# Kernel optimization log

Measured on AMD Instinct MI355X. Metric: run time of the kernel, lower is better.

The kernel has to match this reference:

```python
import jax, jax.numpy as jnp
import numpy as np

EMBED_DIM = 64
N_POINTS = 1_000_000


def sinusoidal_embedding(vals, embed_dim):
    # vals: [B] float -> [B, embed_dim]
    half = embed_dim // 2
    log_scale = np.log(10000.0) / (half - 1)
    freqs = jnp.exp(jnp.arange(half, dtype=jnp.float32) * (-log_scale))
    ang = vals[:, None] * freqs[None, :]
    return jnp.concatenate([jnp.sin(ang), jnp.cos(ang)], axis=1)


def embed_mlp(x, w1, b1, w2, b2):
    # Linear -> LeakyReLU(0.1) -> Linear  (embedf / embedm)
    h = jax.nn.leaky_relu(x @ w1.T + b1, negative_slope=0.1)
    return h @ w2.T + b2


def setup_inputs() -> dict:
    key = jax.random.key(0)
    ks = jax.random.split(key, 12)
    d, dh = EMBED_DIM, EMBED_DIM // 2
    s = lambda fan_in: 1.0 / np.sqrt(fan_in)
    return {
        "inputs": jax.random.normal(ks[0], (1, 6, N_POINTS), dtype=jnp.float32),
        "t": jax.random.uniform(ks[1], (1,), dtype=jnp.float32) * 1000.0,
        "mask": jax.random.randint(ks[2], (N_POINTS,), 0, 2, dtype=jnp.int32),
        "pdf": jax.random.normal(ks[3], (N_POINTS, d), dtype=jnp.float32),
        # embedf params: Linear(d,d), Linear(d,d//2)
        "ef_w1": jax.random.uniform(ks[4], (d, d), minval=-s(d), maxval=s(d)),
        "ef_b1": jnp.zeros((d,), jnp.float32),
        "ef_w2": jax.random.uniform(ks[5], (dh, d), minval=-s(d), maxval=s(d)),
        "ef_b2": jnp.zeros((dh,), jnp.float32),
        # embedm params
        "em_w1": jax.random.uniform(ks[6], (d, d), minval=-s(d), maxval=s(d)),
        "em_b1": jnp.zeros((d,), jnp.float32),
        "em_w2": jax.random.uniform(ks[7], (dh, d), minval=-s(d), maxval=s(d)),
        "em_b2": jnp.zeros((dh,), jnp.float32),
    }


def reference(inputs, t, mask, pdf, ef_w1, ef_b1, ef_w2, ef_b2, em_w1, em_b1, em_w2, em_b2):
    n = inputs.shape[-1]
    # pdf branch: [N, 64] -> [1, 64, N]
    pdf_cnl = pdf.T[None]  # [1, 64, N]
    # timestep embedding -> embedf -> broadcast over points
    te = embed_mlp(sinusoidal_embedding(t, EMBED_DIM), ef_w1, ef_b1, ef_w2, ef_b2)  # [1, 32]
    temb = jnp.broadcast_to(te[:, :, None], (te.shape[0], te.shape[1], n))  # [1, 32, N]
    # per-point mask embedding -> embedm
    me = embed_mlp(sinusoidal_embedding(mask.astype(jnp.float32), EMBED_DIM), em_w1, em_b1, em_w2, em_b2)  # [N, 32]
    memb = me.T[None]  # [1, 32, N]
    temb = jnp.concatenate([temb, memb], axis=1)  # [1, 64, N]
    # return conditioning tensors produced by the (truncated) forward prefix
    return jnp.concatenate([pdf_cnl, temb], axis=1)  # [1, 128, N]
```

## Files before the change

kernel.cpp:

```cpp
#include <hip/hip_runtime.h>
#include <math.h>


#define HALF 32

__global__ void embed_small_kernel(const float* __restrict__ t,
                                   const float* __restrict__ ef_w1, const float* __restrict__ ef_b1,
                                   const float* __restrict__ ef_w2, const float* __restrict__ ef_b2,
                                   const float* __restrict__ em_w1, const float* __restrict__ em_b1,
                                   const float* __restrict__ em_w2, const float* __restrict__ em_b2,
                                   float* __restrict__ ws) {
    __shared__ float h[3][64];
    const int tid = threadIdx.x;
    const float log_scale = 0.2970934777f;

    if (tid < 192) {
        const int v = tid / 64;
        const int j = tid % 64;
        const float val = (v == 0) ? t[0] : (float)(v - 1);
        const float* w1 = (v == 0) ? ef_w1 : em_w1;
        const float* b1 = (v == 0) ? ef_b1 : em_b1;
        float acc = b1[j];
        for (int k = 0; k < HALF; ++k) {
            float f = expf(-(float)k * log_scale);
            float ang = val * f;
            float s, c;
            sincosf(ang, &s, &c);
            acc += s * w1[j * 64 + k] + c * w1[j * 64 + HALF + k];
        }
        h[v][j] = (acc > 0.0f) ? acc : 0.1f * acc;
    }
    __syncthreads();
    if (tid < 96) {
        const int v = tid / 32;
        const int c = tid % 32;
        const float* w2 = (v == 0) ? ef_w2 : em_w2;
        const float* b2 = (v == 0) ? ef_b2 : em_b2;
        float acc = b2[c];
        const float* hh = h[v];
        for (int j = 0; j < 64; ++j) acc += hh[j] * w2[c * 64 + j];
        ws[v * 32 + c] = acc;
    }
}

__global__ __launch_bounds__(256) void pvcnn_cond_kernel(
        const float* __restrict__ pdf,
        const int* __restrict__ mask,
        const float* __restrict__ ws,
        float* __restrict__ out,
        int N) {
    __shared__ float tile[64][65];
    __shared__ float emb[96];

    const int tid = threadIdx.x;
    const long long p0 = (long long)blockIdx.x * 64;
    const bool full = (p0 + 64 <= (long long)N);

    if (tid < 96) emb[tid] = ws[tid];

    if (full) {
        const float4* pdf4 = (const float4*)(pdf + p0 * 64);
        #pragma unroll
        for (int it = 0; it < 4; ++it) {
            int f = tid + it * 256;
            int p = f >> 4;
            int q = f & 15;
            float4 v = pdf4[p * 16 + q];
            tile[p][4 * q + 0] = v.x;
            tile[p][4 * q + 1] = v.y;
            tile[p][4 * q + 2] = v.z;
            tile[p][4 * q + 3] = v.w;
        }
    } else {
        #pragma unroll
        for (int it = 0; it < 4; ++it) {
            int f = tid + it * 256;
            int p = f >> 4;
            int q = f & 15;
            float4 v = make_float4(0.f, 0.f, 0.f, 0.f);
            if (p0 + p < (long long)N) {
                const float4* pdf4 = (const float4*)(pdf + (p0 + p) * 64);
                v = pdf4[q];
            }
            tile[p][4 * q + 0] = v.x;
            tile[p][4 * q + 1] = v.y;
            tile[p][4 * q + 2] = v.z;
            tile[p][4 * q + 3] = v.w;
        }
    }

    const int p = tid & 63;
    const int wv = tid >> 6;
    const bool pok = (p0 + p < (long long)N);
    int mval = 0;
    if (pok) mval = mask[p0 + p];

    __syncthreads();

    if (pok) {
        const long long col = p0 + p;
        #pragma unroll
        for (int cb = 0; cb < 64; cb += 4) {
            int c = cb + wv;
            out[(long long)c * N + col] = tile[p][c];
        }
        #pragma unroll
        for (int cb = 0; cb < 32; cb += 4) {
            int c = cb + wv;
            out[(long long)(64 + c) * N + col] = emb[c];
        }
        #pragma unroll
        for (int cb = 0; cb < 32; cb += 4) {
            int c = cb + wv;
            out[(long long)(96 + c) * N + col] = mval ? emb[64 + c] : emb[32 + c];
        }
    }
}

extern "C" void kernel_launch(void* const* d_in, const int* in_sizes, int n_in,
                              void* d_out, int out_size, void* d_ws, size_t ws_size,
                              hipStream_t stream) {
    const float* t     = (const float*)d_in[1];
    const int*   mask  = (const int*)d_in[2];
    const float* pdf   = (const float*)d_in[3];
    const float* ef_w1 = (const float*)d_in[4];
    const float* ef_b1 = (const float*)d_in[5];
    const float* ef_w2 = (const float*)d_in[6];
    const float* ef_b2 = (const float*)d_in[7];
    const float* em_w1 = (const float*)d_in[8];
    const float* em_b1 = (const float*)d_in[9];
    const float* em_w2 = (const float*)d_in[10];
    const float* em_b2 = (const float*)d_in[11];

    float* out = (float*)d_out;
    float* ws  = (float*)d_ws;
    const int N = in_sizes[2];

    embed_small_kernel<<<1, 192, 0, stream>>>(t, ef_w1, ef_b1, ef_w2, ef_b2,
                                              em_w1, em_b1, em_w2, em_b2, ws);

    const int nblocks = (N + 63) / 64;
    pvcnn_cond_kernel<<<nblocks, 256, 0, stream>>>(pdf, mask, ws, out, N);
}
```

Measured before the change: 163.2 us.

## Widen transpose tile to 256 points and emit float4 stores per row

Each block now handles 256 points instead of 64. The pdf tile uses a padded column-major LDS layout so that each thread can read 4 consecutive points of a channel as a float4. Output writes, and the mask reads on the fast path, become 128-bit vector accesses, so the store-bound transpose issues fewer, wider memory transactions. LDS use per block grows to about 64KB, which lowers occupancy, and a scalar fallback path is kept for tails and for N not divisible by 4.

```diff
diff --git a/kernel.cpp b/kernel.cpp
--- a/kernel.cpp
+++ b/kernel.cpp
@@ -3,6 +3,12 @@
 
 
 #define HALF 32
+#define TS 256
+
+__device__ __forceinline__ int ldsIdx(int c, int p) {
+    return c * 256 + ((c >> 3) << 2) + p;
+}
+#define TILE_FLOATS 16412
 
 __global__ void embed_small_kernel(const float* __restrict__ t,
                                    const float* __restrict__ ef_w1, const float* __restrict__ ef_b1,
@@ -15,8 +21,8 @@
     const float log_scale = 0.2970934777f;
 
     if (tid < 192) {
-        const int v = tid / 64;
-        const int j = tid % 64;
+        const int v = tid >> 6;
+        const int j = tid & 63;
         const float val = (v == 0) ? t[0] : (float)(v - 1);
         const float* w1 = (v == 0) ? ef_w1 : em_w1;
         const float* b1 = (v == 0) ? ef_b1 : em_b1;
@@ -32,13 +38,12 @@
     }
     __syncthreads();
     if (tid < 96) {
-        const int v = tid / 32;
-        const int c = tid % 32;
+        const int v = tid >> 5;
+        const int c = tid & 31;
         const float* w2 = (v == 0) ? ef_w2 : em_w2;
         const float* b2 = (v == 0) ? ef_b2 : em_b2;
         float acc = b2[c];
-        const float* hh = h[v];
-        for (int j = 0; j < 64; ++j) acc += hh[j] * w2[c * 64 + j];
+        for (int j = 0; j < 64; ++j) acc += h[v][j] * w2[c * 64 + j];
         ws[v * 32 + c] = acc;
     }
 }
@@ -49,70 +54,106 @@
         const float* __restrict__ ws,
         float* __restrict__ out,
         int N) {
-    __shared__ float tile[64][65];
+    __shared__ float tile[TILE_FLOATS];
     __shared__ float emb[96];
 
     const int tid = threadIdx.x;
-    const long long p0 = (long long)blockIdx.x * 64;
-    const bool full = (p0 + 64 <= (long long)N);
+    const long long p0 = (long long)blockIdx.x * TS;
+    const bool fast = (p0 + TS <= (long long)N) && ((N & 3) == 0);
 
     if (tid < 96) emb[tid] = ws[tid];
 
-    if (full) {
-        const float4* pdf4 = (const float4*)(pdf + p0 * 64);
+    if (fast) {
+        const float4* src = (const float4*)(pdf + p0 * 64);
         #pragma unroll
-        for (int it = 0; it < 4; ++it) {
-            int f = tid + it * 256;
-            int p = f >> 4;
-            int q = f & 15;
-            float4 v = pdf4[p * 16 + q];
-            tile[p][4 * q + 0] = v.x;
-            tile[p][4 * q + 1] = v.y;
-            tile[p][4 * q + 2] = v.z;
-            tile[p][4 * q + 3] = v.w;
+        for (int it = 0; it < 16; ++it) {
+            const int f = tid + it * 256;
+            const int p = f >> 4;
+            const int c0 = (f & 15) * 4;
+            const float4 v = src[f];
+            const int b = ldsIdx(c0, p);
+            tile[b + 0 * 256] = v.x;
+            tile[b + 1 * 256] = v.y;
+            tile[b + 2 * 256] = v.z;
+            tile[b + 3 * 256] = v.w;
         }
     } else {
         #pragma unroll
-        for (int it = 0; it < 4; ++it) {
-            int f = tid + it * 256;
-            int p = f >> 4;
-            int q = f & 15;
+        for (int it = 0; it < 16; ++it) {
+            const int f = tid + it * 256;
+            const int p = f >> 4;
+            const int c0 = (f & 15) * 4;
             float4 v = make_float4(0.f, 0.f, 0.f, 0.f);
-            if (p0 + p < (long long)N) {
-                const float4* pdf4 = (const float4*)(pdf + (p0 + p) * 64);
-                v = pdf4[q];
-            }
-            tile[p][4 * q + 0] = v.x;
-            tile[p][4 * q + 1] = v.y;
-            tile[p][4 * q + 2] = v.z;
-            tile[p][4 * q + 3] = v.w;
+            if (p0 + p < (long long)N)
+                v = ((const float4*)(pdf + (p0 + p) * 64))[f & 15];
+            const int b = ldsIdx(c0, p);
+            tile[b + 0 * 256] = v.x;
+            tile[b + 1 * 256] = v.y;
+            tile[b + 2 * 256] = v.z;
+            tile[b + 3 * 256] = v.w;
         }
     }
 
-    const int p = tid & 63;
-    const int wv = tid >> 6;
-    const bool pok = (p0 + p < (long long)N);
-    int mval = 0;
-    if (pok) mval = mask[p0 + p];
+    const int l = tid & 63;
+    const int w = tid >> 6;
+    const long long col = p0 + 4 * l;
+
+    int4 m4 = make_int4(0, 0, 0, 0);
+    if (fast) {
+        m4 = ((const int4*)mask)[(p0 >> 2) + l];
+    } else {
+        if (col + 0 < N) m4.x = mask[col + 0];
+        if (col + 1 < N) m4.y = mask[col + 1];
+        if (col + 2 < N) m4.z = mask[col + 2];
+        if (col + 3 < N) m4.w = mask[col + 3];
+    }
 
     __syncthreads();
 
-    if (pok) {
-        const long long col = p0 + p;
+    if (fast) {
+        float* op = out + (long long)w * N + col;
+        const long long stride = 4LL * N;
         #pragma unroll
-        for (int cb = 0; cb < 64; cb += 4) {
-            int c = cb + wv;
-            out[(long long)c * N + col] = tile[p][c];
+        for (int s = 0; s < 32; ++s) {
+            const int r = 4 * s + w;
+            float4 v;
+            if (s < 16) {
+                v = *(const float4*)&tile[ldsIdx(r, 4 * l)];
+            } else if (s < 24) {
+                const float e = emb[r - 64];
+                v = make_float4(e, e, e, e);
+            } else {
+                const int c = r - 96;
+                const float e0 = emb[32 + c];
+                const float e1 = emb[64 + c];
+                v = make_float4(m4.x ? e1 : e0, m4.y ? e1 : e0,
+                                m4.z ? e1 : e0, m4.w ? e1 : e0);
+            }
+            *(float4*)(op + (long long)s * stride) = v;
         }
-        #pragma unroll
-        for (int cb = 0; cb < 32; cb += 4) {
-            int c = cb + wv;
-            out[(long long)(64 + c) * N + col] = emb[c];
-        }
-        #pragma unroll
-        for (int cb = 0; cb < 32; cb += 4) {
-            int c = cb + wv;
-            out[(long long)(96 + c) * N + col] = mval ? emb[64 + c] : emb[32 + c];
+    } else {
+        for (int s = 0; s < 32; ++s) {
+            const int r = 4 * s + w;
+            float vals[4];
+            if (s < 16) {
+                #pragma unroll
+                for (int j = 0; j < 4; ++j) vals[j] = tile[ldsIdx(r, 4 * l + j)];
+            } else if (s < 24) {
+                const float e = emb[r - 64];
+                vals[0] = vals[1] = vals[2] = vals[3] = e;
+            } else {
+                const int c = r - 96;
+                const float e0 = emb[32 + c];
+                const float e1 = emb[64 + c];
+                vals[0] = m4.x ? e1 : e0;
+                vals[1] = m4.y ? e1 : e0;
+                vals[2] = m4.z ? e1 : e0;
+                vals[3] = m4.w ? e1 : e0;
+            }
+            #pragma unroll
+            for (int j = 0; j < 4; ++j)
+                if (col + j < (long long)N)
+                    out[(long long)r * N + col + j] = vals[j];
         }
     }
 }
@@ -139,6 +180,6 @@
     embed_small_kernel<<<1, 192, 0, stream>>>(t, ef_w1, ef_b1, ef_w2, ef_b2,
                                               em_w1, em_b1, em_w2, em_b2, ws);
 
-    const int nblocks = (N + 63) / 64;
+    const int nblocks = (N + TS - 1) / TS;
     pvcnn_cond_kernel<<<nblocks, 256, 0, stream>>>(pdf, mask, ws, out, N);
 }
```

Result: slower. 169.9 us (+4.1%).
